# Kernel optimization log

Measured on AMD Instinct MI355X. Metric: run time of the kernel, lower is better.

## Reference

```python
import jax, jax.numpy as jnp
import numpy as np

B, N, D, H = 4096, 64, 32, 64

def setup_inputs() -> dict:
    key = jax.random.key(0)
    ks = jax.random.split(key, 10)
    s = lambda fan_in: 1.0 / np.sqrt(fan_in)
    return {
        "joint_features": jax.random.normal(ks[0], (B, N, D), jnp.float32),
        "Wm1": jax.random.uniform(ks[1], (2 * D, H), jnp.float32, -s(2 * D), s(2 * D)),
        "bm1": jax.random.uniform(ks[2], (H,), jnp.float32, -s(2 * D), s(2 * D)),
        "Wm2": jax.random.uniform(ks[3], (H, D), jnp.float32, -s(H), s(H)),
        "bm2": jax.random.uniform(ks[4], (D,), jnp.float32, -s(H), s(H)),
        "Wu1": jax.random.uniform(ks[5], (2 * D, H), jnp.float32, -s(2 * D), s(2 * D)),
        "bu1": jax.random.uniform(ks[6], (H,), jnp.float32, -s(2 * D), s(2 * D)),
        "Wu2": jax.random.uniform(ks[7], (H, D), jnp.float32, -s(H), s(H)),
        "bu2": jax.random.uniform(ks[8], (D,), jnp.float32, -s(H), s(H)),
        "residual_weight": jnp.float32(0.5),
        "num_joints": N,
    }

def reference(joint_features, Wm1, bm1, Wm2, bm2, Wu1, bu1, Wu2, bu2, residual_weight, num_joints):
    n = num_joints
    # chain topology: directed edges (i->i+1) and (i+1->i); dst receives message
    dst = jnp.concatenate([jnp.arange(n - 1), jnp.arange(1, n)])  # [E]
    src = jnp.concatenate([jnp.arange(1, n), jnp.arange(n - 1)])  # [E]
    # edge gather + concat: [B, E, 2D]
    edge_in = jnp.concatenate([joint_features[:, dst], joint_features[:, src]], axis=-1)
    # message MLP (ReLU after both layers, per original Sequential)
    msg = jax.nn.relu(jax.nn.relu(edge_in @ Wm1 + bm1) @ Wm2 + bm2)  # [B, E, D]
    # scatter-add messages to destination nodes
    messages = jnp.zeros_like(joint_features).at[:, dst].add(msg)  # [B, N, D]
    # per-node update MLP on concat(feature, message)
    upd_in = jnp.concatenate([joint_features, messages], axis=-1)  # [B, N, 2D]
    updated = jax.nn.relu(upd_in @ Wu1 + bu1) @ Wu2 + bu2  # [B, N, D]
    return residual_weight * updated + (1.0 - residual_weight) * joint_features
```

## Files before the change

### kernel.cpp

```cpp
#include <hip/hip_runtime.h>
#include <hip/hip_bf16.h>


typedef __bf16 bf16x8 __attribute__((ext_vector_type(8)));
typedef float  f32x4  __attribute__((ext_vector_type(4)));
typedef unsigned short u16;

#define NBATCH 8
#define NBI 2
#define ITERS (NBATCH / NBI)
#define HS  72
#define MBS 40

__device__ __forceinline__ u16 f2b(float f) { return __builtin_bit_cast(u16, (__bf16)f); }
__device__ __forceinline__ f32x4 MFMA(bf16x8 a, bf16x8 b, f32x4 c) {
    return __builtin_amdgcn_mfma_f32_16x16x32_bf16(a, b, c, 0, 0, 0);
}
__device__ __forceinline__ bf16x8 pack8(float4 a, float4 b) {
    bf16x8 r = {(__bf16)a.x, (__bf16)a.y, (__bf16)a.z, (__bf16)a.w,
                (__bf16)b.x, (__bf16)b.y, (__bf16)b.z, (__bf16)b.w};
    return r;
}
__device__ __forceinline__ uint2 relu_pack4(f32x4 acc, f32x4 bias) {
    uint2 o;
    o.x = (unsigned)f2b(fmaxf(acc[0] + bias[0], 0.f)) |
          ((unsigned)f2b(fmaxf(acc[1] + bias[1], 0.f)) << 16);
    o.y = (unsigned)f2b(fmaxf(acc[2] + bias[2], 0.f)) |
          ((unsigned)f2b(fmaxf(acc[3] + bias[3], 0.f)) << 16);
    return o;
}
__device__ __forceinline__ void wave_lds_fence() {
    asm volatile("s_waitcnt lgkmcnt(0)" ::: "memory");
}
__device__ __forceinline__ void barrier_lds() {
    asm volatile("s_waitcnt lgkmcnt(0)" ::: "memory");
    __builtin_amdgcn_s_barrier();
    asm volatile("" ::: "memory");
}

__global__ __launch_bounds__(256, 2)
void agn_mfma(const float* __restrict__ x, const float* __restrict__ Wm1,
              const float* __restrict__ bm1, const float* __restrict__ Wm2,
              const float* __restrict__ bm2, const float* __restrict__ Wu1,
              const float* __restrict__ bu1, const float* __restrict__ Wu2,
              const float* __restrict__ bu2, const float* __restrict__ rw_p,
              float* __restrict__ out)
{
    __shared__ __align__(16) u16 sH[256 * HS];
    __shared__ __align__(16) u16 sMB[256 * MBS];

    const int t = threadIdx.x;
    const int w = t >> 6;
    const int lane = t & 63;
    const int ln = lane & 15;
    const int q  = lane >> 4;

    bf16x8 B1a[4], B1b[4], B2[2][2], B3[2][4], B4[2][2];
#pragma unroll
    for (int nt = 0; nt < 4; ++nt)
#pragma unroll
        for (int j = 0; j < 8; ++j) {
            B1a[nt][j] = (__bf16)Wm1[(q * 8 + j) * 64 + nt * 16 + ln];
            B1b[nt][j] = (__bf16)Wm1[(32 + q * 8 + j) * 64 + nt * 16 + ln];
        }
#pragma unroll
    for (int s = 0; s < 2; ++s)
#pragma unroll
        for (int nt = 0; nt < 2; ++nt)
#pragma unroll
            for (int j = 0; j < 8; ++j)
                B2[s][nt][j] = (__bf16)Wm2[(s * 32 + q * 8 + j) * 32 + nt * 16 + ln];
#pragma unroll
    for (int s = 0; s < 2; ++s)
#pragma unroll
        for (int nt = 0; nt < 4; ++nt)
#pragma unroll
            for (int j = 0; j < 8; ++j)
                B3[s][nt][j] = (__bf16)Wu1[(s * 32 + q * 8 + j) * 64 + nt * 16 + ln];
#pragma unroll
    for (int s = 0; s < 2; ++s)
#pragma unroll
        for (int nt = 0; nt < 2; ++nt)
#pragma unroll
            for (int j = 0; j < 8; ++j)
                B4[s][nt][j] = (__bf16)Wu2[(s * 32 + q * 8 + j) * 32 + nt * 16 + ln];

    f32x4 bm1s[4], bu1s[4], bm2s[2];
#pragma unroll
    for (int ht = 0; ht < 4; ++ht)
#pragma unroll
        for (int r = 0; r < 4; ++r) {
            bm1s[ht][r] = bm1[ht * 16 + q * 4 + r];
            bu1s[ht][r] = bu1[ht * 16 + q * 4 + r];
        }
#pragma unroll
    for (int s = 0; s < 2; ++s)
#pragma unroll
        for (int r = 0; r < 4; ++r)
            bm2s[s][r] = bm2[s * 16 + q * 4 + r];
    float bu2v[2];
#pragma unroll
    for (int nt = 0; nt < 2; ++nt) bu2v[nt] = bu2[nt * 16 + ln];
    const float rw = rw_p[0];
    const float om = 1.f - rw;

    const size_t base = (size_t)blockIdx.x * (NBATCH * 64 * 32);

    for (int it = 0; it < ITERS; ++it) {
        const float* xit = x + base + (size_t)it * (NBI * 64 * 32);
        float*       oit = out + base + (size_t)it * (NBI * 64 * 32);

        {
            float4 xd[4][2], xsv[4][2];
#pragma unroll
            for (int m = 0; m < 4; ++m) {
                const int et = 4 * w + m;
                const int erow = et * 16 + ln;
                const int bb = erow >> 7;
                int e = erow & 127;
                if (e >= 126) e = 0;
                const int dst  = (e < 63) ? e : e - 62;
                const int srcn = (e < 63) ? e + 1 : e - 63;
                const float* pd = xit + ((bb << 6) + dst) * 32 + q * 8;
                const float* ps = xit + ((bb << 6) + srcn) * 32 + q * 8;
                xd[m][0] = *(const float4*)pd;  xd[m][1] = *(const float4*)(pd + 4);
                xsv[m][0] = *(const float4*)ps; xsv[m][1] = *(const float4*)(ps + 4);
            }
#pragma unroll
            for (int m = 0; m < 4; ++m) {
                const int erow = (4 * w + m) * 16 + ln;
                bf16x8 Ad = pack8(xd[m][0], xd[m][1]);
                bf16x8 As = pack8(xsv[m][0], xsv[m][1]);
                u16* rowp = &sH[erow * HS];
#pragma unroll
                for (int ht = 0; ht < 4; ++ht) {
                    f32x4 acc = {0.f, 0.f, 0.f, 0.f};
                    acc = MFMA(B1a[ht], Ad, acc);
                    acc = MFMA(B1b[ht], As, acc);
                    *(uint2*)&rowp[ht * 16 + q * 4] = relu_pack4(acc, bm1s[ht]);
                }
            }
        }
        wave_lds_fence();

#pragma unroll
        for (int m = 0; m < 4; ++m) {
            const int row = (4 * w + m) * 16 + ln;
            bf16x8 A0 = __builtin_bit_cast(bf16x8, *(const uint4*)&sH[row * HS + q * 8]);
            bf16x8 A1 = __builtin_bit_cast(bf16x8, *(const uint4*)&sH[row * HS + 32 + q * 8]);
#pragma unroll
            for (int s = 0; s < 2; ++s) {
                f32x4 acc = {0.f, 0.f, 0.f, 0.f};
                acc = MFMA(B2[0][s], A0, acc);
                acc = MFMA(B2[1][s], A1, acc);
                *(uint2*)&sMB[row * MBS + s * 16 + q * 4] = relu_pack4(acc, bm2s[s]);
            }
        }
        barrier_lds();

#pragma unroll
        for (int m = 0; m < 2; ++m) {
            const int row = (2 * w + m) * 16 + ln;
            const int bb = row >> 6;
            const int i2 = row & 63;
            const float* p = xit + row * 32 + q * 8;
            float4 a0 = *(const float4*)p;
            float4 a1 = *(const float4*)(p + 4);
            bf16x8 A0 = pack8(a0, a1);
            float mv[8] = {0.f, 0.f, 0.f, 0.f, 0.f, 0.f, 0.f, 0.f};
            if (i2 < 63) {
                uint4 u = *(const uint4*)&sMB[((bb << 7) + i2) * MBS + q * 8];
                const unsigned* pu = (const unsigned*)&u;
#pragma unroll
                for (int h = 0; h < 4; ++h) {
                    mv[2 * h]     += __uint_as_float(pu[h] << 16);
                    mv[2 * h + 1] += __uint_as_float(pu[h] & 0xFFFF0000u);
                }
            }
            if (i2 > 0) {
                uint4 u = *(const uint4*)&sMB[((bb << 7) + 62 + i2) * MBS + q * 8];
                const unsigned* pu = (const unsigned*)&u;
#pragma unroll
                for (int h = 0; h < 4; ++h) {
                    mv[2 * h]     += __uint_as_float(pu[h] << 16);
                    mv[2 * h + 1] += __uint_as_float(pu[h] & 0xFFFF0000u);
                }
            }
            bf16x8 A1;
#pragma unroll
            for (int j = 0; j < 8; ++j) A1[j] = (__bf16)mv[j];
#pragma unroll
            for (int ht = 0; ht < 4; ++ht) {
                f32x4 acc = {0.f, 0.f, 0.f, 0.f};
                acc = MFMA(B3[0][ht], A0, acc);
                acc = MFMA(B3[1][ht], A1, acc);
                *(uint2*)&sH[row * HS + ht * 16 + q * 4] = relu_pack4(acc, bu1s[ht]);
            }
        }
        wave_lds_fence();

#pragma unroll
        for (int m = 0; m < 2; ++m) {
            const int mt = 2 * w + m;
            const int arow = mt * 16 + ln;
            bf16x8 A0 = __builtin_bit_cast(bf16x8, *(const uint4*)&sH[arow * HS + q * 8]);
            bf16x8 A1 = __builtin_bit_cast(bf16x8, *(const uint4*)&sH[arow * HS + 32 + q * 8]);
#pragma unroll
            for (int nt = 0; nt < 2; ++nt) {
                f32x4 acc = {0.f, 0.f, 0.f, 0.f};
                acc = MFMA(A0, B4[0][nt], acc);
                acc = MFMA(A1, B4[1][nt], acc);
                const int rb = mt * 16 + q * 4;
                const int c  = nt * 16 + ln;
#pragma unroll
                for (int r = 0; r < 4; ++r) {
                    const int off = (rb + r) * 32 + c;
                    oit[off] = rw * (acc[r] + bu2v[nt]) + om * xit[off];
                }
            }
        }
        barrier_lds();
    }
}

extern "C" void kernel_launch(void* const* d_in, const int* in_sizes, int n_in,
                              void* d_out, int out_size, void* d_ws, size_t ws_size,
                              hipStream_t stream) {
    const float* x   = (const float*)d_in[0];
    const float* Wm1 = (const float*)d_in[1];
    const float* bm1 = (const float*)d_in[2];
    const float* Wm2 = (const float*)d_in[3];
    const float* bm2 = (const float*)d_in[4];
    const float* Wu1 = (const float*)d_in[5];
    const float* bu1 = (const float*)d_in[6];
    const float* Wu2 = (const float*)d_in[7];
    const float* bu2 = (const float*)d_in[8];
    const float* rw  = (const float*)d_in[9];
    float* out = (float*)d_out;

    const int B = in_sizes[0] / (64 * 32);
    agn_mfma<<<B / NBATCH, 256, 0, stream>>>(x, Wm1, bm1, Wm2, bm2, Wu1, bu1, Wu2, bu2, rw, out);
}
```

Before: 124.2 us.

## Process one batch per iteration with four batches per block and higher occupancy

Each block iteration now handles a single batch element instead of two, halving per-iteration work per wave, the LDS buffers and the unrolled loops. Each block covers four batches instead of eight, so the grid presumably doubles, and launch bounds now ask for four blocks per CU. The aim is more resident waves to hide global memory latency. The cost is that the per-block setup, including loading weights into registers, is amortized over fewer batches, and register pressure is capped more tightly.

```diff
diff --git a/kernel.cpp b/kernel.cpp
--- a/kernel.cpp
+++ b/kernel.cpp
@@ -6,9 +6,8 @@
 typedef float  f32x4  __attribute__((ext_vector_type(4)));
 typedef unsigned short u16;
 
-#define NBATCH 8
-#define NBI 2
-#define ITERS (NBATCH / NBI)
+#define NBATCH 4
+#define ITERS  NBATCH
 #define HS  72
 #define MBS 40
 
@@ -38,7 +37,7 @@
     asm volatile("" ::: "memory");
 }
 
-__global__ __launch_bounds__(256, 2)
+__global__ __launch_bounds__(256, 4)
 void agn_mfma(const float* __restrict__ x, const float* __restrict__ Wm1,
               const float* __restrict__ bm1, const float* __restrict__ Wm2,
               const float* __restrict__ bm2, const float* __restrict__ Wu1,
@@ -46,8 +45,8 @@
               const float* __restrict__ bu2, const float* __restrict__ rw_p,
               float* __restrict__ out)
 {
-    __shared__ __align__(16) u16 sH[256 * HS];
-    __shared__ __align__(16) u16 sMB[256 * MBS];
+    __shared__ __align__(16) u16 sH[128 * HS];
+    __shared__ __align__(16) u16 sMB[128 * MBS];
 
     const int t = threadIdx.x;
     const int w = t >> 6;
@@ -107,28 +106,26 @@
     const size_t base = (size_t)blockIdx.x * (NBATCH * 64 * 32);
 
     for (int it = 0; it < ITERS; ++it) {
-        const float* xit = x + base + (size_t)it * (NBI * 64 * 32);
-        float*       oit = out + base + (size_t)it * (NBI * 64 * 32);
+        const float* xit = x + base + (size_t)it * (64 * 32);
+        float*       oit = out + base + (size_t)it * (64 * 32);
 
         {
-            float4 xd[4][2], xsv[4][2];
-#pragma unroll
-            for (int m = 0; m < 4; ++m) {
-                const int et = 4 * w + m;
-                const int erow = et * 16 + ln;
-                const int bb = erow >> 7;
-                int e = erow & 127;
+            float4 xd[2][2], xsv[2][2];
+#pragma unroll
+            for (int m = 0; m < 2; ++m) {
+                const int erow = (2 * w + m) * 16 + ln;
+                int e = erow;
                 if (e >= 126) e = 0;
                 const int dst  = (e < 63) ? e : e - 62;
                 const int srcn = (e < 63) ? e + 1 : e - 63;
-                const float* pd = xit + ((bb << 6) + dst) * 32 + q * 8;
-                const float* ps = xit + ((bb << 6) + srcn) * 32 + q * 8;
+                const float* pd = xit + dst * 32 + q * 8;
+                const float* ps = xit + srcn * 32 + q * 8;
                 xd[m][0] = *(const float4*)pd;  xd[m][1] = *(const float4*)(pd + 4);
                 xsv[m][0] = *(const float4*)ps; xsv[m][1] = *(const float4*)(ps + 4);
             }
 #pragma unroll
-            for (int m = 0; m < 4; ++m) {
-                const int erow = (4 * w + m) * 16 + ln;
+            for (int m = 0; m < 2; ++m) {
+                const int erow = (2 * w + m) * 16 + ln;
                 bf16x8 Ad = pack8(xd[m][0], xd[m][1]);
                 bf16x8 As = pack8(xsv[m][0], xsv[m][1]);
                 u16* rowp = &sH[erow * HS];
@@ -144,8 +141,8 @@
         wave_lds_fence();
 
 #pragma unroll
-        for (int m = 0; m < 4; ++m) {
-            const int row = (4 * w + m) * 16 + ln;
+        for (int m = 0; m < 2; ++m) {
+            const int row = (2 * w + m) * 16 + ln;
             bf16x8 A0 = __builtin_bit_cast(bf16x8, *(const uint4*)&sH[row * HS + q * 8]);
             bf16x8 A1 = __builtin_bit_cast(bf16x8, *(const uint4*)&sH[row * HS + 32 + q * 8]);
 #pragma unroll
@@ -158,18 +155,15 @@
         }
         barrier_lds();
 
-#pragma unroll
-        for (int m = 0; m < 2; ++m) {
-            const int row = (2 * w + m) * 16 + ln;
-            const int bb = row >> 6;
-            const int i2 = row & 63;
+        {
+            const int row = w * 16 + ln;
             const float* p = xit + row * 32 + q * 8;
             float4 a0 = *(const float4*)p;
             float4 a1 = *(const float4*)(p + 4);
             bf16x8 A0 = pack8(a0, a1);
             float mv[8] = {0.f, 0.f, 0.f, 0.f, 0.f, 0.f, 0.f, 0.f};
-            if (i2 < 63) {
-                uint4 u = *(const uint4*)&sMB[((bb << 7) + i2) * MBS + q * 8];
+            if (row < 63) {
+                uint4 u = *(const uint4*)&sMB[row * MBS + q * 8];
                 const unsigned* pu = (const unsigned*)&u;
 #pragma unroll
                 for (int h = 0; h < 4; ++h) {
@@ -177,8 +171,8 @@
                     mv[2 * h + 1] += __uint_as_float(pu[h] & 0xFFFF0000u);
                 }
             }
-            if (i2 > 0) {
-                uint4 u = *(const uint4*)&sMB[((bb << 7) + 62 + i2) * MBS + q * 8];
+            if (row > 0) {
+                uint4 u = *(const uint4*)&sMB[(62 + row) * MBS + q * 8];
                 const unsigned* pu = (const unsigned*)&u;
 #pragma unroll
                 for (int h = 0; h < 4; ++h) {
@@ -199,10 +193,8 @@
         }
         wave_lds_fence();
 
-#pragma unroll
-        for (int m = 0; m < 2; ++m) {
-            const int mt = 2 * w + m;
-            const int arow = mt * 16 + ln;
+        {
+            const int arow = w * 16 + ln;
             bf16x8 A0 = __builtin_bit_cast(bf16x8, *(const uint4*)&sH[arow * HS + q * 8]);
             bf16x8 A1 = __builtin_bit_cast(bf16x8, *(const uint4*)&sH[arow * HS + 32 + q * 8]);
 #pragma unroll
@@ -210,7 +202,7 @@
                 f32x4 acc = {0.f, 0.f, 0.f, 0.f};
                 acc = MFMA(A0, B4[0][nt], acc);
                 acc = MFMA(A1, B4[1][nt], acc);
-                const int rb = mt * 16 + q * 4;
+                const int rb = w * 16 + q * 4;
                 const int c  = nt * 16 + ln;
 #pragma unroll
                 for (int r = 0; r < 4; ++r) {
```

Result: slower. 186.0 us (+49.8%).

## Stage input tile in LDS and vectorize output stores via transposed final MFMA

Applied to the files above, without the earlier changes.

Each iteration now cooperatively copies the input tile into a padded fp32 LDS buffer with coalesced float4 loads. The edge gather, the update-MLP input and the residual term then read from LDS instead of issuing repeated scattered global loads. The final MFMA swaps its operands so each lane holds four consecutive columns, which allows float4 output stores instead of scalar ones. The cost is an extra barrier per iteration and about 18KB more LDS, which may reduce occupancy.

```diff
diff --git a/kernel.cpp b/kernel.cpp
--- a/kernel.cpp
+++ b/kernel.cpp
@@ -11,6 +11,7 @@
 #define ITERS (NBATCH / NBI)
 #define HS  72
 #define MBS 40
+#define XS  36
 
 __device__ __forceinline__ u16 f2b(float f) { return __builtin_bit_cast(u16, (__bf16)f); }
 __device__ __forceinline__ f32x4 MFMA(bf16x8 a, bf16x8 b, f32x4 c) {
@@ -46,8 +47,9 @@
               const float* __restrict__ bu2, const float* __restrict__ rw_p,
               float* __restrict__ out)
 {
-    __shared__ __align__(16) u16 sH[256 * HS];
-    __shared__ __align__(16) u16 sMB[256 * MBS];
+    __shared__ __align__(16) u16   sH[256 * HS];
+    __shared__ __align__(16) u16   sMB[256 * MBS];
+    __shared__ __align__(16) float sX[128 * XS];
 
     const int t = threadIdx.x;
     const int w = t >> 6;
@@ -85,7 +87,7 @@
             for (int j = 0; j < 8; ++j)
                 B4[s][nt][j] = (__bf16)Wu2[(s * 32 + q * 8 + j) * 32 + nt * 16 + ln];
 
-    f32x4 bm1s[4], bu1s[4], bm2s[2];
+    f32x4 bm1s[4], bu1s[4], bm2s[2], bu2s[2];
 #pragma unroll
     for (int ht = 0; ht < 4; ++ht)
 #pragma unroll
@@ -96,11 +98,10 @@
 #pragma unroll
     for (int s = 0; s < 2; ++s)
 #pragma unroll
-        for (int r = 0; r < 4; ++r)
+        for (int r = 0; r < 4; ++r) {
             bm2s[s][r] = bm2[s * 16 + q * 4 + r];
-    float bu2v[2];
-#pragma unroll
-    for (int nt = 0; nt < 2; ++nt) bu2v[nt] = bu2[nt * 16 + ln];
+            bu2s[s][r] = bu2[s * 16 + q * 4 + r];
+        }
     const float rw = rw_p[0];
     const float om = 1.f - rw;
 
@@ -111,34 +112,44 @@
         float*       oit = out + base + (size_t)it * (NBI * 64 * 32);
 
         {
-            float4 xd[4][2], xsv[4][2];
-#pragma unroll
-            for (int m = 0; m < 4; ++m) {
-                const int et = 4 * w + m;
-                const int erow = et * 16 + ln;
-                const int bb = erow >> 7;
-                int e = erow & 127;
-                if (e >= 126) e = 0;
-                const int dst  = (e < 63) ? e : e - 62;
-                const int srcn = (e < 63) ? e + 1 : e - 63;
-                const float* pd = xit + ((bb << 6) + dst) * 32 + q * 8;
-                const float* ps = xit + ((bb << 6) + srcn) * 32 + q * 8;
-                xd[m][0] = *(const float4*)pd;  xd[m][1] = *(const float4*)(pd + 4);
-                xsv[m][0] = *(const float4*)ps; xsv[m][1] = *(const float4*)(ps + 4);
-            }
-#pragma unroll
-            for (int m = 0; m < 4; ++m) {
-                const int erow = (4 * w + m) * 16 + ln;
-                bf16x8 Ad = pack8(xd[m][0], xd[m][1]);
-                bf16x8 As = pack8(xsv[m][0], xsv[m][1]);
-                u16* rowp = &sH[erow * HS];
-#pragma unroll
-                for (int ht = 0; ht < 4; ++ht) {
-                    f32x4 acc = {0.f, 0.f, 0.f, 0.f};
-                    acc = MFMA(B1a[ht], Ad, acc);
-                    acc = MFMA(B1b[ht], As, acc);
-                    *(uint2*)&rowp[ht * 16 + q * 4] = relu_pack4(acc, bm1s[ht]);
-                }
+            const int row = t >> 1;
+            const int cb  = (t & 1) * 16;
+            const float* src = xit + row * 32 + cb;
+            float* dstp = &sX[row * XS + cb];
+            float4 v0 = *(const float4*)(src);
+            float4 v1 = *(const float4*)(src + 4);
+            float4 v2 = *(const float4*)(src + 8);
+            float4 v3 = *(const float4*)(src + 12);
+            *(float4*)(dstp)      = v0;
+            *(float4*)(dstp + 4)  = v1;
+            *(float4*)(dstp + 8)  = v2;
+            *(float4*)(dstp + 12) = v3;
+        }
+        barrier_lds();
+
+#pragma unroll
+        for (int m = 0; m < 4; ++m) {
+            const int erow = (4 * w + m) * 16 + ln;
+            const int bb = erow >> 7;
+            int e = erow & 127;
+            if (e >= 126) e = 0;
+            const int dst  = (e < 63) ? e : e - 62;
+            const int srcn = (e < 63) ? e + 1 : e - 63;
+            const float* pd = &sX[((bb << 6) + dst) * XS + q * 8];
+            const float* ps = &sX[((bb << 6) + srcn) * XS + q * 8];
+            float4 d0 = *(const float4*)pd;
+            float4 d1 = *(const float4*)(pd + 4);
+            float4 s0 = *(const float4*)ps;
+            float4 s1 = *(const float4*)(ps + 4);
+            bf16x8 Ad = pack8(d0, d1);
+            bf16x8 As = pack8(s0, s1);
+            u16* rowp = &sH[erow * HS];
+#pragma unroll
+            for (int ht = 0; ht < 4; ++ht) {
+                f32x4 acc = {0.f, 0.f, 0.f, 0.f};
+                acc = MFMA(B1a[ht], Ad, acc);
+                acc = MFMA(B1b[ht], As, acc);
+                *(uint2*)&rowp[ht * 16 + q * 4] = relu_pack4(acc, bm1s[ht]);
             }
         }
         wave_lds_fence();
@@ -163,7 +174,7 @@
             const int row = (2 * w + m) * 16 + ln;
             const int bb = row >> 6;
             const int i2 = row & 63;
-            const float* p = xit + row * 32 + q * 8;
+            const float* p = &sX[row * XS + q * 8];
             float4 a0 = *(const float4*)p;
             float4 a1 = *(const float4*)(p + 4);
             bf16x8 A0 = pack8(a0, a1);
@@ -201,22 +212,21 @@
 
 #pragma unroll
         for (int m = 0; m < 2; ++m) {
-            const int mt = 2 * w + m;
-            const int arow = mt * 16 + ln;
-            bf16x8 A0 = __builtin_bit_cast(bf16x8, *(const uint4*)&sH[arow * HS + q * 8]);
-            bf16x8 A1 = __builtin_bit_cast(bf16x8, *(const uint4*)&sH[arow * HS + 32 + q * 8]);
-#pragma unroll
-            for (int nt = 0; nt < 2; ++nt) {
-                f32x4 acc = {0.f, 0.f, 0.f, 0.f};
-                acc = MFMA(A0, B4[0][nt], acc);
-                acc = MFMA(A1, B4[1][nt], acc);
-                const int rb = mt * 16 + q * 4;
-                const int c  = nt * 16 + ln;
-#pragma unroll
-                for (int r = 0; r < 4; ++r) {
-                    const int off = (rb + r) * 32 + c;
-                    oit[off] = rw * (acc[r] + bu2v[nt]) + om * xit[off];
-                }
+            const int row = (2 * w + m) * 16 + ln;
+            bf16x8 A0 = __builtin_bit_cast(bf16x8, *(const uint4*)&sH[row * HS + q * 8]);
+            bf16x8 A1 = __builtin_bit_cast(bf16x8, *(const uint4*)&sH[row * HS + 32 + q * 8]);
+#pragma unroll
+            for (int s = 0; s < 2; ++s) {
+                f32x4 acc = {0.f, 0.f, 0.f, 0.f};
+                acc = MFMA(B4[0][s], A0, acc);
+                acc = MFMA(B4[1][s], A1, acc);
+                f32x4 xv = *(const f32x4*)&sX[row * XS + s * 16 + q * 4];
+                float4 o;
+                o.x = rw * (acc[0] + bu2s[s][0]) + om * xv[0];
+                o.y = rw * (acc[1] + bu2s[s][1]) + om * xv[1];
+                o.z = rw * (acc[2] + bu2s[s][2]) + om * xv[2];
+                o.w = rw * (acc[3] + bu2s[s][3]) + om * xv[3];
+                *(float4*)(oit + row * 32 + s * 16 + q * 4) = o;
             }
         }
         barrier_lds();
```

Result: faster. 117.7 us (-5.2%).
